# Kernel tuning notes

Hardware: AMD Instinct MI355X
Metric: run time of the kernel (lower is better)

Reference implementation:

```python
import jax, jax.numpy as jnp
import numpy as np

NEG_SLOPE = 0.2  # PyG GATConv default leaky_relu slope


def gat_layer(x, src, dst, W, a_src, a_dst, bias, heads, d, concat):
    # x: [N, in_dim]; src/dst: [E] (edges flow src -> dst, self-loops included)
    N = x.shape[0]
    h = (x @ W).reshape(N, heads, d)                      # [N, H, D]
    alpha_src = jnp.einsum('nhd,hd->nh', h, a_src)        # [N, H]
    alpha_dst = jnp.einsum('nhd,hd->nh', h, a_dst)        # [N, H]
    e = jax.nn.leaky_relu(alpha_src[src] + alpha_dst[dst], NEG_SLOPE)  # [E, H]
    # softmax over incoming edges of each destination node (segment softmax)
    m = jax.ops.segment_max(e, dst, num_segments=N)       # [N, H]
    ex = jnp.exp(e - m[dst])
    s = jax.ops.segment_sum(ex, dst, num_segments=N)      # [N, H]
    alpha = ex / s[dst]                                   # [E, H]
    msg = h[src] * alpha[..., None]                       # [E, H, D]
    out = jax.ops.segment_sum(msg, dst, num_segments=N)   # [N, H, D]
    out = out.reshape(N, heads * d) if concat else out.mean(axis=1)
    return out + bias


def setup_inputs() -> dict:
    key = jax.random.key(0)
    ks = jax.random.split(key, 12)
    N, E = 10000, 320000
    in_dim, hidden, heads, out_dim = 256, 64, 4, 40
    x = jax.random.normal(ks[0], (N, in_dim), dtype=jnp.float32)
    edge_index = jax.random.randint(ks[1], (2, E), 0, N, dtype=jnp.int64)
    s = 0.1
    return {
        'x': x,
        'edge_index': edge_index,
        'W1': jax.random.normal(ks[2], (in_dim, heads * hidden), jnp.float32) * s,
        'att_src1': jax.random.normal(ks[3], (heads, hidden), jnp.float32) * s,
        'att_dst1': jax.random.normal(ks[4], (heads, hidden), jnp.float32) * s,
        'bias1': jnp.zeros((heads * hidden,), jnp.float32),
        'W2': jax.random.normal(ks[5], (heads * hidden, out_dim), jnp.float32) * s,
        'att_src2': jax.random.normal(ks[6], (1, out_dim), jnp.float32) * s,
        'att_dst2': jax.random.normal(ks[7], (1, out_dim), jnp.float32) * s,
        'bias2': jnp.zeros((out_dim,), jnp.float32),
    }


def reference(x, edge_index, W1, att_src1, att_dst1, bias1, W2, att_src2, att_dst2, bias2):
    N = x.shape[0]
    # PyG GATConv adds self-loops by default
    loop = jnp.arange(N, dtype=edge_index.dtype)
    src = jnp.concatenate([edge_index[0], loop])
    dst = jnp.concatenate([edge_index[1], loop])
    h = gat_layer(x, src, dst, W1, att_src1, att_dst1, bias1, heads=4, d=64, concat=True)
    h = jax.nn.relu(h)
    out = gat_layer(h, src, dst, W2, att_src2, att_dst2, bias2, heads=1, d=40, concat=False)
    return jax.nn.log_softmax(out, axis=1)
```

## Files before the change

kernel.cpp:

```cpp
#include <hip/hip_runtime.h>
#include <hip/hip_bf16.h>
#include <math.h>

#define IN_DIM 256
#define C1 256
#define H1 4
#define OUT_DIM 40
#define W2PAD 48
#define NEG_SLOPE 0.2f
#define DSTRIDE 128

typedef __attribute__((ext_vector_type(8))) short bf16x8;
typedef __attribute__((ext_vector_type(4))) float f32x4;
typedef __attribute__((ext_vector_type(2))) float f32x2;

#define XS_LD 264

__device__ __forceinline__ unsigned short f2bf(float f) {
    union { float f; unsigned u; } c; c.f = f;
    unsigned r = c.u + 0x7fffu + ((c.u >> 16) & 1u);
    return (unsigned short)(r >> 16);
}

__device__ __forceinline__ unsigned char f2fp8(float f) {
    return (unsigned char)__builtin_amdgcn_cvt_pk_fp8_f32(f, 0.f, 0, false);
}

__device__ __forceinline__ float sel4(float4 v, int h) {
    float r = v.x;
    r = (h == 1) ? v.y : r;
    r = (h == 2) ? v.z : r;
    r = (h == 3) ? v.w : r;
    return r;
}

__device__ __forceinline__ float leaky(float v) {
    return (v >= 0.0f) ? v : NEG_SLOPE * v;
}

__global__ void k_prep(int* __restrict__ fill, const float* __restrict__ W1,
                       unsigned short* __restrict__ W1t, const float* __restrict__ W2,
                       unsigned short* __restrict__ W2t, const float* __restrict__ a_src2,
                       const float* __restrict__ a_dst2, float* __restrict__ w2s,
                       float* __restrict__ w2d, int N) {
    int t = threadIdx.x;
    int g = blockIdx.x * 256 + t;
    if (g < N) fill[g << 4] = 0;
    if (g < C1) {
        float s = 0.0f, d = 0.0f;
#pragma unroll
        for (int j = 0; j < OUT_DIM; ++j) {
            float w = W2[g * OUT_DIM + j];
            s += w * a_src2[j];
            d += w * a_dst2[j];
        }
        w2s[g] = s;
        w2d[g] = d;
    }
    if (g < W2PAD * C1) {
        int j = g >> 8, k = g & 255;
        W2t[g] = (j < OUT_DIM) ? f2bf(W2[k * OUT_DIM + j]) : 0;
    }
    __shared__ float s32[32][33];
    int b = blockIdx.x;
    int r0 = (b >> 3) * 32;
    int c0 = (b & 7) * 32;
    for (int i = t; i < 1024; i += 256) {
        int lr = i >> 5, lc = i & 31;
        s32[lr][lc] = W1[(r0 + lr) * 256 + c0 + lc];
    }
    __syncthreads();
    for (int i = t; i < 1024; i += 256) {
        int oc = i >> 5, ok = i & 31;
        W1t[(c0 + oc) * 256 + r0 + ok] = f2bf(s32[ok][oc]);
    }
}

__global__ void __launch_bounds__(256) k_fused1(
    const float* __restrict__ x, const unsigned short* __restrict__ W1t,
    const float* __restrict__ a_src, const float* __restrict__ a_dst,
    unsigned char* __restrict__ h1, float* __restrict__ as1, float* __restrict__ ad1,
    const int* __restrict__ ei, int* __restrict__ fill, unsigned short* __restrict__ srcs,
    int N, int E, int ET, int G1) {
    __shared__ unsigned short xs[64 * XS_LD];
    int t = threadIdx.x;

    if (blockIdx.x >= G1) {
        int eb = (blockIdx.x - G1) * 1024 + t;
#pragma unroll
        for (int k = 0; k < 4; ++k) {
            int e = eb + k * 256;
            if (e < ET) {
                int s, d;
                if (e < E) { s = ei[e]; d = ei[E + e]; }
                else       { s = e - E; d = s; }
                int pos = atomicAdd(&fill[d << 4], 1);
                srcs[(d << 7) + pos] = (unsigned short)s;
            }
        }
        return;
    }

    int n0 = blockIdx.x * 64;
    for (int i = t; i < 4096; i += 256) {
        int r = i >> 6, c4 = i & 63;
        int n = n0 + r;
        float4 v = (n < N) ? ((const float4*)x)[(size_t)n * 64 + c4]
                           : make_float4(0.f, 0.f, 0.f, 0.f);
        uint2 pk;
        pk.x = (unsigned)f2bf(v.x) | ((unsigned)f2bf(v.y) << 16);
        pk.y = (unsigned)f2bf(v.z) | ((unsigned)f2bf(v.w) << 16);
        *((uint2*)&xs[r * XS_LD + c4 * 4]) = pk;
    }
    __syncthreads();

    int wv = t >> 6, lane = t & 63;
    int quad = lane >> 4, ln = lane & 15;

    f32x4 acc[4][4];
#pragma unroll
    for (int mt = 0; mt < 4; ++mt)
#pragma unroll
        for (int nt = 0; nt < 4; ++nt) acc[mt][nt] = (f32x4){0.f, 0.f, 0.f, 0.f};

#pragma unroll
    for (int kb = 0; kb < 8; ++kb) {
        bf16x8 af[4], bf[4];
#pragma unroll
        for (int mt = 0; mt < 4; ++mt)
            af[mt] = *((bf16x8*)&xs[(mt * 16 + ln) * XS_LD + kb * 32 + quad * 8]);
#pragma unroll
        for (int nt = 0; nt < 4; ++nt)
            bf[nt] = *((const bf16x8*)(W1t + ((wv * 64 + nt * 16 + ln) * 256 + kb * 32 + quad * 8)));
#pragma unroll
        for (int mt = 0; mt < 4; ++mt)
#pragma unroll
            for (int nt = 0; nt < 4; ++nt)
                acc[mt][nt] = __builtin_amdgcn_mfma_f32_16x16x32_bf16(af[mt], bf[nt], acc[mt][nt], 0, 0, 0);
    }

    float asv[4], adv[4];
#pragma unroll
    for (int nt = 0; nt < 4; ++nt) {
        int col = wv * 64 + nt * 16 + ln;
        asv[nt] = a_src[col];
        adv[nt] = a_dst[col];
    }
#pragma unroll
    for (int mt = 0; mt < 4; ++mt) {
        float ds[4] = {0.f, 0.f, 0.f, 0.f};
        float dd[4] = {0.f, 0.f, 0.f, 0.f};
#pragma unroll
        for (int nt = 0; nt < 4; ++nt) {
#pragma unroll
            for (int r = 0; r < 4; ++r) {
                float v = acc[mt][nt][r];
                ds[r] += v * asv[nt];
                dd[r] += v * adv[nt];
            }
        }
#pragma unroll
        for (int r = 0; r < 4; ++r) {
            float vs = ds[r], vd = dd[r];
#pragma unroll
            for (int o = 1; o < 16; o <<= 1) {
                vs += __shfl_xor(vs, o);
                vd += __shfl_xor(vd, o);
            }
            if (ln == 0) {
                int node = n0 + mt * 16 + quad * 4 + r;
                if (node < N) {
                    as1[node * H1 + wv] = vs;
                    ad1[node * H1 + wv] = vd;
                }
            }
        }
    }

    __syncthreads();
    unsigned char* bt = (unsigned char*)xs;
#pragma unroll
    for (int mt = 0; mt < 4; ++mt)
#pragma unroll
        for (int nt = 0; nt < 4; ++nt)
#pragma unroll
            for (int r = 0; r < 4; ++r)
                bt[(mt * 16 + quad * 4 + r) * 256 + wv * 64 + nt * 16 + ln] = f2fp8(acc[mt][nt][r]);
    __syncthreads();
    const uint4* bt4 = (const uint4*)bt;
    uint4* h14 = (uint4*)(h1 + (size_t)n0 * C1);
    for (int i = t; i < 1024; i += 256) {
        int row = i >> 4;
        if (n0 + row < N) h14[i] = bt4[i];
    }
}

__global__ void __launch_bounds__(256) k_node1(
    const int* __restrict__ fill, const unsigned short* __restrict__ srcs,
    const float* __restrict__ as1f, const float* __restrict__ ad1f,
    const unsigned char* __restrict__ h1, const float* __restrict__ bias1,
    const float* __restrict__ w2s, const float* __restrict__ w2d,
    const unsigned short* __restrict__ W2t, unsigned short* __restrict__ h2b,
    float* __restrict__ as2, float* __restrict__ ad2, int N) {
    int w = threadIdx.x >> 6, lane = threadIdx.x & 63;
    int n = blockIdx.x * 4 + w;
    bool valid = (n < N);
    __shared__ float4 es[4][64];
    __shared__ unsigned short Abuf[16 * 256];
    int start = n << 7;
    int end = start + (valid ? fill[n << 4] : 0);
    const float4* as4 = (const float4*)as1f;
    float4 adn = valid ? ((const float4*)ad1f)[n] : make_float4(0.f, 0.f, 0.f, 0.f);
    int h = lane >> 4;
    const float* esw = (const float*)&es[w][0];

    float4 S4 = make_float4(0.f, 0.f, 0.f, 0.f);
    float ac0 = 0.f, ac1 = 0.f, ac2 = 0.f, ac3 = 0.f;

    for (int c = start; c < end; c += 64) {
        int cnt = min(64, end - c);
        int idx = c + lane;
        int sreg = (idx < end) ? (int)srcs[idx] : 0;
        float4 ex = make_float4(0.f, 0.f, 0.f, 0.f);
        if (idx < end) {
            float4 a = as4[sreg];
            ex.x = __expf(leaky(a.x + adn.x));
            ex.y = __expf(leaky(a.y + adn.y));
            ex.z = __expf(leaky(a.z + adn.z));
            ex.w = __expf(leaky(a.w + adn.w));
        }
        S4.x += ex.x; S4.y += ex.y; S4.z += ex.z; S4.w += ex.w;
        es[w][lane] = ex;

        int i = 0;
        for (; i + 7 < cnt; i += 8) {
            int s[8]; float a[8]; unsigned r[8];
#pragma unroll
            for (int k = 0; k < 8; ++k) {
                s[k] = __shfl(sreg, i + k);
                a[k] = esw[(i + k) * 4 + h];
            }
#pragma unroll
            for (int k = 0; k < 8; ++k)
                r[k] = ((const unsigned*)(h1 + (size_t)s[k] * C1))[lane];
#pragma unroll
            for (int k = 0; k < 8; ++k) {
                f32x2 lo = __builtin_amdgcn_cvt_pk_f32_fp8(r[k], false);
                f32x2 hi = __builtin_amdgcn_cvt_pk_f32_fp8(r[k], true);
                ac0 += a[k] * lo.x;
                ac1 += a[k] * lo.y;
                ac2 += a[k] * hi.x;
                ac3 += a[k] * hi.y;
            }
        }
        for (; i < cnt; ++i) {
            int s0 = __shfl(sreg, i);
            float a0 = esw[i * 4 + h];
            unsigned r0 = ((const unsigned*)(h1 + (size_t)s0 * C1))[lane];
            f32x2 lo = __builtin_amdgcn_cvt_pk_f32_fp8(r0, false);
            f32x2 hi = __builtin_amdgcn_cvt_pk_f32_fp8(r0, true);
            ac0 += a0 * lo.x;
            ac1 += a0 * lo.y;
            ac2 += a0 * hi.x;
            ac3 += a0 * hi.y;
        }
    }

#pragma unroll
    for (int o = 32; o > 0; o >>= 1) {
        S4.x += __shfl_xor(S4.x, o);
        S4.y += __shfl_xor(S4.y, o);
        S4.z += __shfl_xor(S4.z, o);
        S4.w += __shfl_xor(S4.w, o);
    }
    float iS = 1.0f / sel4(S4, h);
    float4 b = ((const float4*)bias1)[lane];
    float v0 = fmaxf(ac0 * iS + b.x, 0.f);
    float v1 = fmaxf(ac1 * iS + b.y, 0.f);
    float v2 = fmaxf(ac2 * iS + b.z, 0.f);
    float v3 = fmaxf(ac3 * iS + b.w, 0.f);
    uint2 pk;
    pk.x = (unsigned)f2bf(v0) | ((unsigned)f2bf(v1) << 16);
    pk.y = (unsigned)f2bf(v2) | ((unsigned)f2bf(v3) << 16);
    ((uint2*)&Abuf[w * 256])[lane] = pk;

    float4 ws = ((const float4*)w2s)[lane];
    float4 wd = ((const float4*)w2d)[lane];
    float ps = v0 * ws.x + v1 * ws.y + v2 * ws.z + v3 * ws.w;
    float pd = v0 * wd.x + v1 * wd.y + v2 * wd.z + v3 * wd.w;
#pragma unroll
    for (int o = 32; o > 0; o >>= 1) {
        ps += __shfl_xor(ps, o);
        pd += __shfl_xor(pd, o);
    }
    if (lane == 0 && valid) { as2[n] = ps; ad2[n] = pd; }

    __syncthreads();
    if (w < 3) {
        int quad = lane >> 4, ln = lane & 15;
        f32x4 acc = (f32x4){0.f, 0.f, 0.f, 0.f};
        const unsigned short* bbase = W2t + (w * 16 + ln) * 256;
#pragma unroll
        for (int kb = 0; kb < 8; ++kb) {
            bf16x8 af = *((bf16x8*)&Abuf[ln * 256 + kb * 32 + quad * 8]);
            bf16x8 bfr = *((const bf16x8*)(bbase + kb * 32 + quad * 8));
            acc = __builtin_amdgcn_mfma_f32_16x16x32_bf16(af, bfr, acc, 0, 0, 0);
        }
        int col = w * 16 + ln;
        if (col < OUT_DIM && quad == 0) {
#pragma unroll
            for (int r = 0; r < 4; ++r) {
                int node = blockIdx.x * 4 + r;
                if (node < N) h2b[(size_t)node * OUT_DIM + col] = f2bf(acc[r]);
            }
        }
    }
}

__global__ void __launch_bounds__(256) k_node2(
    const int* __restrict__ fill, const unsigned short* __restrict__ srcs,
    const float* __restrict__ as2, const float* __restrict__ ad2,
    const unsigned short* __restrict__ h2b, const float* __restrict__ bias2,
    float* __restrict__ out, int N) {
    int w = threadIdx.x >> 6, lane = threadIdx.x & 63;
    int n = blockIdx.x * 4 + w;
    if (n >= N) return;
    int start = n << 7;
    int end = start + fill[n << 4];
    float adn = ad2[n];
    float S = 0.f, acc0 = 0.f, acc1 = 0.f;
    bool act = lane < 20;

    for (int c = start; c < end; c += 64) {
        int cnt = min(64, end - c);
        int idx = c + lane;
        int sreg = (idx < end) ? (int)srcs[idx] : 0;
        float ex = (idx < end) ? __expf(leaky(as2[sreg] + adn)) : 0.f;
        S += ex;
        int i = 0;
        for (; i + 3 < cnt; i += 4) {
            int su[4]; float al[4]; unsigned rw[4];
#pragma unroll
            for (int k = 0; k < 4; ++k) {
                su[k] = __shfl(sreg, i + k);
                al[k] = __shfl(ex, i + k);
            }
#pragma unroll
            for (int k = 0; k < 4; ++k)
                rw[k] = act ? *(const unsigned*)(h2b + (size_t)su[k] * OUT_DIM + lane * 2) : 0u;
#pragma unroll
            for (int k = 0; k < 4; ++k) {
                acc0 += al[k] * __uint_as_float(rw[k] << 16);
                acc1 += al[k] * __uint_as_float(rw[k] & 0xffff0000u);
            }
        }
        for (; i < cnt; ++i) {
            int su0 = __shfl(sreg, i);
            float al0 = __shfl(ex, i);
            unsigned rw0 = act ? *(const unsigned*)(h2b + (size_t)su0 * OUT_DIM + lane * 2) : 0u;
            acc0 += al0 * __uint_as_float(rw0 << 16);
            acc1 += al0 * __uint_as_float(rw0 & 0xffff0000u);
        }
    }
#pragma unroll
    for (int o = 32; o > 0; o >>= 1) S += __shfl_xor(S, o);

    float v0 = act ? (acc0 / S + bias2[lane * 2]) : -INFINITY;
    float v1 = act ? (acc1 / S + bias2[lane * 2 + 1]) : -INFINITY;
    float mx = fmaxf(v0, v1);
#pragma unroll
    for (int o = 16; o > 0; o >>= 1) mx = fmaxf(mx, __shfl_xor(mx, o));
    float e0 = act ? __expf(v0 - mx) : 0.f;
    float e1 = act ? __expf(v1 - mx) : 0.f;
    float esum = e0 + e1;
#pragma unroll
    for (int o = 16; o > 0; o >>= 1) esum += __shfl_xor(esum, o);
    if (act) {
        float l = mx + logf(esum);
        out[(size_t)n * OUT_DIM + lane * 2]     = v0 - l;
        out[(size_t)n * OUT_DIM + lane * 2 + 1] = v1 - l;
    }
}

extern "C" void kernel_launch(void* const* d_in, const int* in_sizes, int n_in,
                              void* d_out, int out_size, void* d_ws, size_t ws_size,
                              hipStream_t stream) {
    const float* x        = (const float*)d_in[0];
    const int*   ei       = (const int*)d_in[1];
    const float* W1       = (const float*)d_in[2];
    const float* att_src1 = (const float*)d_in[3];
    const float* att_dst1 = (const float*)d_in[4];
    const float* bias1    = (const float*)d_in[5];
    const float* W2       = (const float*)d_in[6];
    const float* att_src2 = (const float*)d_in[7];
    const float* att_dst2 = (const float*)d_in[8];
    const float* bias2    = (const float*)d_in[9];
    float* out = (float*)d_out;

    const int N  = in_sizes[0] / IN_DIM;
    const int E  = in_sizes[1] / 2;
    const int ET = E + N;

    char* base = (char*)d_ws;
    auto alloc = [&](size_t bytes) {
        char* p = base;
        base += (bytes + 255) & ~(size_t)255;
        return p;
    };
    unsigned char*  h1    = (unsigned char*)alloc((size_t)N * C1);
    unsigned short* W1t   = (unsigned short*)alloc((size_t)C1 * C1 * 2);
    unsigned short* W2t   = (unsigned short*)alloc((size_t)W2PAD * C1 * 2);
    unsigned short* h2b   = (unsigned short*)alloc((size_t)N * OUT_DIM * 2);
    float* as1   = (float*)alloc((size_t)N * H1 * 4);
    float* ad1   = (float*)alloc((size_t)N * H1 * 4);
    float* as2   = (float*)alloc((size_t)N * 4);
    float* ad2   = (float*)alloc((size_t)N * 4);
    float* w2s   = (float*)alloc((size_t)C1 * 4);
    float* w2d   = (float*)alloc((size_t)C1 * 4);
    int* fill    = (int*)alloc((size_t)N * 16 * 4);
    unsigned short* srcs = (unsigned short*)alloc((size_t)N * DSTRIDE * 2);

    const int G1 = (N + 63) / 64;
    const int GS = (ET + 1023) / 1024;

    k_prep<<<64, 256, 0, stream>>>(fill, W1, W1t, W2, W2t, att_src2, att_dst2, w2s, w2d, N);
    k_fused1<<<G1 + GS, 256, 0, stream>>>(x, W1t, att_src1, att_dst1, h1, as1, ad1,
                                          ei, fill, srcs, N, E, ET, G1);
    k_node1<<<(N + 3) / 4, 256, 0, stream>>>(fill, srcs, as1, ad1, h1, bias1, w2s, w2d,
                                             W2t, h2b, as2, ad2, N);
    k_node2<<<(N + 3) / 4, 256, 0, stream>>>(fill, srcs, as2, ad2, h2b, bias2, out, N);
}
```

Before: 141.5 us.

## Bank edge-bucket atomics per XCC and split scatter from GEMM kernel

```diff
diff --git a/kernel.cpp b/kernel.cpp
--- a/kernel.cpp
+++ b/kernel.cpp
@@ -8,7 +8,8 @@
 #define OUT_DIM 40
 #define W2PAD 48
 #define NEG_SLOPE 0.2f
-#define DSTRIDE 128
+#define NBANK 8
+#define BSLOT 128
 
 typedef __attribute__((ext_vector_type(8))) short bf16x8;
 typedef __attribute__((ext_vector_type(4))) float f32x4;
@@ -38,14 +39,20 @@
     return (v >= 0.0f) ? v : NEG_SLOPE * v;
 }
 
-__global__ void k_prep(int* __restrict__ fill, const float* __restrict__ W1,
+__device__ __forceinline__ int xcc_id() {
+    int x;
+    asm volatile("s_getreg_b32 %0, hwreg(HW_REG_XCC_ID)" : "=s"(x));
+    return x & (NBANK - 1);
+}
+
+__global__ void k_prep(int* __restrict__ fill2, const float* __restrict__ W1,
                        unsigned short* __restrict__ W1t, const float* __restrict__ W2,
                        unsigned short* __restrict__ W2t, const float* __restrict__ a_src2,
                        const float* __restrict__ a_dst2, float* __restrict__ w2s,
                        float* __restrict__ w2d, int N) {
     int t = threadIdx.x;
     int g = blockIdx.x * 256 + t;
-    if (g < N) fill[g << 4] = 0;
+    for (int i = g; i < NBANK * N; i += 64 * 256) fill2[i << 4] = 0;
     if (g < C1) {
         float s = 0.0f, d = 0.0f;
 #pragma unroll
@@ -76,31 +83,32 @@
     }
 }
 
-__global__ void __launch_bounds__(256) k_fused1(
+__global__ void __launch_bounds__(256) k_scatter(
+    const int* __restrict__ ei, int* __restrict__ fill2, unsigned short* __restrict__ srcs2,
+    int N, int E, int ET) {
+    int t = threadIdx.x;
+    int xb = xcc_id() * N;
+    int eb = blockIdx.x * 1024 + t;
+#pragma unroll
+    for (int k = 0; k < 4; ++k) {
+        int e = eb + k * 256;
+        if (e < ET) {
+            int s, d;
+            if (e < E) { s = ei[e]; d = ei[E + e]; }
+            else       { s = e - E; d = s; }
+            int pos = atomicAdd(&fill2[(xb + d) << 4], 1);
+            srcs2[(size_t)(xb + d) * BSLOT + pos] = (unsigned short)s;
+        }
+    }
+}
+
+__global__ void __launch_bounds__(256) k_gemm1(
     const float* __restrict__ x, const unsigned short* __restrict__ W1t,
     const float* __restrict__ a_src, const float* __restrict__ a_dst,
     unsigned char* __restrict__ h1, float* __restrict__ as1, float* __restrict__ ad1,
-    const int* __restrict__ ei, int* __restrict__ fill, unsigned short* __restrict__ srcs,
-    int N, int E, int ET, int G1) {
+    int N) {
     __shared__ unsigned short xs[64 * XS_LD];
     int t = threadIdx.x;
-
-    if (blockIdx.x >= G1) {
-        int eb = (blockIdx.x - G1) * 1024 + t;
-#pragma unroll
-        for (int k = 0; k < 4; ++k) {
-            int e = eb + k * 256;
-            if (e < ET) {
-                int s, d;
-                if (e < E) { s = ei[e]; d = ei[E + e]; }
-                else       { s = e - E; d = s; }
-                int pos = atomicAdd(&fill[d << 4], 1);
-                srcs[(d << 7) + pos] = (unsigned short)s;
-            }
-        }
-        return;
-    }
-
     int n0 = blockIdx.x * 64;
     for (int i = t; i < 4096; i += 256) {
         int r = i >> 6, c4 = i & 63;
@@ -196,7 +204,7 @@
 }
 
 __global__ void __launch_bounds__(256) k_node1(
-    const int* __restrict__ fill, const unsigned short* __restrict__ srcs,
+    const int* __restrict__ fill2, const unsigned short* __restrict__ srcs2,
     const float* __restrict__ as1f, const float* __restrict__ ad1f,
     const unsigned char* __restrict__ h1, const float* __restrict__ bias1,
     const float* __restrict__ w2s, const float* __restrict__ w2d,
@@ -207,8 +215,14 @@
     bool valid = (n < N);
     __shared__ float4 es[4][64];
     __shared__ unsigned short Abuf[16 * 256];
-    int start = n << 7;
-    int end = start + (valid ? fill[n << 4] : 0);
+
+    int off[NBANK + 1];
+    off[0] = 0;
+#pragma unroll
+    for (int b = 0; b < NBANK; ++b)
+        off[b + 1] = off[b] + (valid ? fill2[(b * N + n) << 4] : 0);
+    int deg = off[NBANK];
+
     const float4* as4 = (const float4*)as1f;
     float4 adn = valid ? ((const float4*)ad1f)[n] : make_float4(0.f, 0.f, 0.f, 0.f);
     int h = lane >> 4;
@@ -217,12 +231,19 @@
     float4 S4 = make_float4(0.f, 0.f, 0.f, 0.f);
     float ac0 = 0.f, ac1 = 0.f, ac2 = 0.f, ac3 = 0.f;
 
-    for (int c = start; c < end; c += 64) {
-        int cnt = min(64, end - c);
+    for (int c = 0; c < deg; c += 64) {
+        int cnt = min(64, deg - c);
         int idx = c + lane;
-        int sreg = (idx < end) ? (int)srcs[idx] : 0;
+        int sreg = 0;
+        if (idx < deg) {
+            int jj = 0, bo = 0;
+#pragma unroll
+            for (int j = 1; j < NBANK; ++j)
+                if (idx >= off[j]) { jj = j; bo = off[j]; }
+            sreg = (int)srcs2[(size_t)(jj * N + n) * BSLOT + (idx - bo)];
+        }
         float4 ex = make_float4(0.f, 0.f, 0.f, 0.f);
-        if (idx < end) {
+        if (idx < deg) {
             float4 a = as4[sreg];
             ex.x = __expf(leaky(a.x + adn.x));
             ex.y = __expf(leaky(a.y + adn.y));
@@ -318,24 +339,37 @@
 }
 
 __global__ void __launch_bounds__(256) k_node2(
-    const int* __restrict__ fill, const unsigned short* __restrict__ srcs,
+    const int* __restrict__ fill2, const unsigned short* __restrict__ srcs2,
     const float* __restrict__ as2, const float* __restrict__ ad2,
     const unsigned short* __restrict__ h2b, const float* __restrict__ bias2,
     float* __restrict__ out, int N) {
     int w = threadIdx.x >> 6, lane = threadIdx.x & 63;
     int n = blockIdx.x * 4 + w;
     if (n >= N) return;
-    int start = n << 7;
-    int end = start + fill[n << 4];
+
+    int off[NBANK + 1];
+    off[0] = 0;
+#pragma unroll
+    for (int b = 0; b < NBANK; ++b)
+        off[b + 1] = off[b] + fill2[(b * N + n) << 4];
+    int deg = off[NBANK];
+
     float adn = ad2[n];
     float S = 0.f, acc0 = 0.f, acc1 = 0.f;
     bool act = lane < 20;
 
-    for (int c = start; c < end; c += 64) {
-        int cnt = min(64, end - c);
+    for (int c = 0; c < deg; c += 64) {
+        int cnt = min(64, deg - c);
         int idx = c + lane;
-        int sreg = (idx < end) ? (int)srcs[idx] : 0;
-        float ex = (idx < end) ? __expf(leaky(as2[sreg] + adn)) : 0.f;
+        int sreg = 0;
+        if (idx < deg) {
+            int jj = 0, bo = 0;
+#pragma unroll
+            for (int j = 1; j < NBANK; ++j)
+                if (idx >= off[j]) { jj = j; bo = off[j]; }
+            sreg = (int)srcs2[(size_t)(jj * N + n) * BSLOT + (idx - bo)];
+        }
+        float ex = (idx < deg) ? __expf(leaky(as2[sreg] + adn)) : 0.f;
         S += ex;
         int i = 0;
         for (; i + 3 < cnt; i += 4) {
@@ -417,16 +451,16 @@
     float* ad2   = (float*)alloc((size_t)N * 4);
     float* w2s   = (float*)alloc((size_t)C1 * 4);
     float* w2d   = (float*)alloc((size_t)C1 * 4);
-    int* fill    = (int*)alloc((size_t)N * 16 * 4);
-    unsigned short* srcs = (unsigned short*)alloc((size_t)N * DSTRIDE * 2);
+    int* fill2   = (int*)alloc((size_t)NBANK * N * 16 * 4);
+    unsigned short* srcs2 = (unsigned short*)alloc((size_t)NBANK * N * BSLOT * 2);
 
     const int G1 = (N + 63) / 64;
     const int GS = (ET + 1023) / 1024;
 
-    k_prep<<<64, 256, 0, stream>>>(fill, W1, W1t, W2, W2t, att_src2, att_dst2, w2s, w2d, N);
-    k_fused1<<<G1 + GS, 256, 0, stream>>>(x, W1t, att_src1, att_dst1, h1, as1, ad1,
-                                          ei, fill, srcs, N, E, ET, G1);
-    k_node1<<<(N + 3) / 4, 256, 0, stream>>>(fill, srcs, as1, ad1, h1, bias1, w2s, w2d,
+    k_prep<<<64, 256, 0, stream>>>(fill2, W1, W1t, W2, W2t, att_src2, att_dst2, w2s, w2d, N);
+    k_scatter<<<GS, 256, 0, stream>>>(ei, fill2, srcs2, N, E, ET);
+    k_gemm1<<<G1, 256, 0, stream>>>(x, W1t, att_src1, att_dst1, h1, as1, ad1, N);
+    k_node1<<<(N + 3) / 4, 256, 0, stream>>>(fill2, srcs2, as1, ad1, h1, bias1, w2s, w2d,
                                              W2t, h2b, as2, ad2, N);
-    k_node2<<<(N + 3) / 4, 256, 0, stream>>>(fill, srcs, as2, ad2, h2b, bias2, out, N);
-}
+    k_node2<<<(N + 3) / 4, 256, 0, stream>>>(fill2, srcs2, as2, ad2, h2b, bias2, out, N);
+}
```

Result: slower. 149.9 us (+5.9%).
